# Kernel optimization log

Measured on AMD Instinct MI355X. Metric: run time of the kernel, lower is better.

The kernel has to match this reference:

```python
import jax, jax.numpy as jnp
import numpy as np

EPS = 1e-12  # torch F.normalize eps

def _l2n(x, axis):
    n = jnp.linalg.norm(x, axis=axis, keepdims=True)
    return x / jnp.maximum(n, EPS)

def setup_inputs() -> dict:
    key = jax.random.key(0)
    ks = jax.random.split(key, 11)
    B, N, D = 8, 4096, 512
    s = 1.0 / np.sqrt(D)
    return {
        'a': jax.random.normal(ks[0], (B, N, D), jnp.float32),
        'b': jax.random.normal(ks[1], (B, N, D), jnp.float32),
        'Wq': jax.random.normal(ks[2], (D, D), jnp.float32) * s,
        'bq': jax.random.normal(ks[3], (D,), jnp.float32) * s,
        'Wk': jax.random.normal(ks[4], (D, D), jnp.float32) * s,
        'bk': jax.random.normal(ks[5], (D,), jnp.float32) * s,
        'w_g': jax.random.normal(ks[6], (D, 1), jnp.float32),
        'Wp': jax.random.normal(ks[7], (D, D), jnp.float32) * s,
        'bp': jax.random.normal(ks[8], (D,), jnp.float32) * s,
        'Wf': jax.random.normal(ks[9], (D, D), jnp.float32) * s,
        'bf': jax.random.normal(ks[10], (D,), jnp.float32) * s,
    }

def reference(a, b, Wq, bq, Wk, bk, w_g, Wp, bp, Wf, bf):
    D = a.shape[-1]
    scale = D ** (-0.5)
    query = _l2n(jnp.einsum('bnd,ed->bne', a, Wq) + bq, axis=-1)   # [B,N,D]
    key = _l2n(jnp.einsum('bnd,ed->bne', b, Wk) + bk, axis=-1)     # [B,N,D]
    A = (query @ w_g) * scale                                      # [B,N,1]
    A = _l2n(A, axis=1)                                            # normalize over seq
    G = jnp.sum(A * query, axis=1)                                 # [B,D] learned pooling
    gk = G[:, None, :] * key                                       # broadcast [B,N,D]
    out = jnp.einsum('bnd,ed->bne', gk, Wp) + bp + query           # residual
    out = jnp.einsum('bnd,ed->bne', out, Wf) + bf
    return out
```

## Files before the change

### kernel.cpp

```cpp
#include <hip/hip_runtime.h>
#include <stdint.h>

#define DD 512
#define MTOT 32768

typedef float f32x4 __attribute__((ext_vector_type(4)));
typedef __bf16 bf16x8 __attribute__((ext_vector_type(8)));

static __device__ __forceinline__ unsigned short f2bf(float f) {
  union { float f; unsigned int u; } c; c.f = f;
  unsigned int r = c.u + 0x7fffu + ((c.u >> 16) & 1u);
  return (unsigned short)(r >> 16);
}
static __device__ __forceinline__ float bf2f(unsigned short h) {
  union { unsigned int u; float f; } c; c.u = ((unsigned int)h) << 16;
  return c.f;
}

union FragU { uint4 u; bf16x8 b; };

static __device__ __forceinline__ void load_lds16(const void* g, void* l) {
  __builtin_amdgcn_global_load_lds(
      (const __attribute__((address_space(1))) void*)g,
      (__attribute__((address_space(3))) void*)l, 16, 0, 0);
}

__global__ __launch_bounds__(256) void cvt3w_k(const float* __restrict__ W0,
    const float* __restrict__ W1, const float* __restrict__ W2,
    unsigned short* __restrict__ D0, unsigned short* __restrict__ D1,
    unsigned short* __restrict__ D2, float* __restrict__ stats) {
  int slab = blockIdx.x >> 8;
  if (slab == 3) {
    int i = ((blockIdx.x - 768) * 256 + threadIdx.x) * 4;
    *(float4*)(stats + i) = make_float4(0.f, 0.f, 0.f, 0.f);
    return;
  }
  int off = ((blockIdx.x & 255) * 256 + threadIdx.x) * 4;
  const float* s = slab == 0 ? W0 : slab == 1 ? W1 : W2;
  unsigned short* d = slab == 0 ? D0 : slab == 1 ? D1 : D2;
  float4 f = *(const float4*)(s + off);
  ushort4 h;
  h.x = f2bf(f.x); h.y = f2bf(f.y); h.z = f2bf(f.z); h.w = f2bf(f.w);
  *(ushort4*)(d + off) = h;
}

__global__ __launch_bounds__(256) void scalew_k(const float* __restrict__ Wp,
    const float* __restrict__ G, unsigned short* __restrict__ out) {
  int i = (blockIdx.x * 256 + threadIdx.x) * 4;
  int b = i >> 18;
  int rem = i & 262143;
  int d = rem & 511;
  float4 w = *(const float4*)(Wp + rem);
  float4 g = *(const float4*)(G + b * DD + d);
  ushort4 h;
  h.x = f2bf(w.x * g.x); h.y = f2bf(w.y * g.y);
  h.z = f2bf(w.z * g.z); h.w = f2bf(w.w * g.w);
  *(ushort4*)(out + i) = h;
}

static __device__ __forceinline__ void gemm_core(
    const unsigned short* __restrict__ X, const unsigned short* __restrict__ W,
    int row0, int col0, unsigned short* As, unsigned short* Bs,
    f32x4 (&acc)[4][4]) {
  const int tid = threadIdx.x;
  const int lane = tid & 63, wave = tid >> 6;
  const int sr = lane >> 3;
  const int scol = ((lane & 7) ^ sr) * 8;
  const unsigned short* Ag = X + (size_t)(row0 + wave * 32 + sr) * DD + scol;
  const unsigned short* Bg = W + (size_t)(col0 + wave * 32 + sr) * DD + scol;
  const int ldsb = wave * 32 * 64;
  const int fr = lane & 15, quad = lane >> 4;
  const int wr = (wave >> 1) * 64, wc = (wave & 1) * 64;
  const int sw0 = ((quad ^ (fr & 7)) * 8);
  const int sw1 = (((quad + 4) ^ (fr & 7)) * 8);

  for (int k0 = 0; k0 < DD; k0 += 64) {
#pragma unroll
    for (int q = 0; q < 4; q++) {
      load_lds16(Ag + (size_t)q * 8 * DD + k0, As + ldsb + q * 8 * 64);
      load_lds16(Bg + (size_t)q * 8 * DD + k0, Bs + ldsb + q * 8 * 64);
    }
    __syncthreads();
#pragma unroll
    for (int kk = 0; kk < 2; kk++) {
      const int sw = kk ? sw1 : sw0;
      bf16x8 af[4], bfr[4];
#pragma unroll
      for (int i = 0; i < 4; i++) {
        FragU u; u.u = *(const uint4*)&As[(wr + i * 16 + fr) * 64 + sw];
        af[i] = u.b;
      }
#pragma unroll
      for (int j = 0; j < 4; j++) {
        FragU u; u.u = *(const uint4*)&Bs[(wc + j * 16 + fr) * 64 + sw];
        bfr[j] = u.b;
      }
#pragma unroll
      for (int i = 0; i < 4; i++)
#pragma unroll
        for (int j = 0; j < 4; j++)
          acc[i][j] = __builtin_amdgcn_mfma_f32_16x16x32_bf16(af[i], bfr[j], acc[i][j], 0, 0, 0);
    }
    __syncthreads();
  }
}

__global__ __launch_bounds__(256) void gemm_qk_k(
    const float* __restrict__ Xa, const float* __restrict__ Xb,
    const unsigned short* __restrict__ Wqw, const unsigned short* __restrict__ Wkw,
    const float* __restrict__ bq, const float* __restrict__ bk,
    const float* __restrict__ wg,
    float* __restrict__ ssqQ, float* __restrict__ ssqK, float* __restrict__ Pdot,
    unsigned short* __restrict__ Cq, unsigned short* __restrict__ Ck) {
  __shared__ float AsF[128 * 64];
  __shared__ unsigned short Bs[128 * 64];
  const int swz = (blockIdx.x & 7) * 256 + (blockIdx.x >> 3);
  const int isK = swz >> 10;
  const int t = swz & 1023;
  const int row0 = (t >> 2) * 128, col0 = (t & 3) * 128;
  const float* X = isK ? Xb : Xa;
  const unsigned short* W = isK ? Wkw : Wqw;
  const float* bias = isK ? bk : bq;
  float* ssq = isK ? ssqK : ssqQ;
  unsigned short* C = isK ? Ck : Cq;

  const int lane = threadIdx.x & 63, wave = threadIdx.x >> 6;

  const int rl = lane >> 4;
  const int gsE = (lane & 15) ^ (rl << 1);
  const int gsO = gsE ^ 1;
  const float* AgE = X + (size_t)(row0 + wave * 32 + rl) * DD + gsE * 4;
  const float* AgO = X + (size_t)(row0 + wave * 32 + rl) * DD + gsO * 4;
  const int ldsA = wave * 2048;

  const int sr = lane >> 3;
  const int scol = ((lane & 7) ^ sr) * 8;
  const unsigned short* Bg = W + (size_t)(col0 + wave * 32 + sr) * DD + scol;
  const int ldsb = wave * 32 * 64;

  const int fr = lane & 15, quad = lane >> 4;
  const int wr = (wave >> 1) * 64, wc = (wave & 1) * 64;
  const int xorv = ((fr & 7) >> 2) | ((fr & 3) << 1);
  const int swB0 = ((quad ^ (fr & 7)) * 8);
  const int swB1 = (((quad + 4) ^ (fr & 7)) * 8);

  f32x4 acc[4][4] = {};

  for (int k0 = 0; k0 < DD; k0 += 64) {
#pragma unroll
    for (int q = 0; q < 8; q++) {
      const float* src = ((q & 1) ? AgO : AgE) + (size_t)q * 4 * DD + k0;
      load_lds16(src, AsF + ldsA + q * 256);
    }
#pragma unroll
    for (int q = 0; q < 4; q++)
      load_lds16(Bg + (size_t)q * 8 * DD + k0, Bs + ldsb + q * 8 * 64);
    __syncthreads();
#pragma unroll
    for (int kk = 0; kk < 2; kk++) {
      const int glo = ((kk * 4 + quad) * 2) ^ xorv;
      const int ghi = glo ^ 1;
      const int swB = kk ? swB1 : swB0;
      bf16x8 af[4], bfr[4];
#pragma unroll
      for (int i = 0; i < 4; i++) {
        const float* ap = &AsF[(wr + i * 16 + fr) * 64];
        f32x4 lo = *(const f32x4*)(ap + glo * 4);
        f32x4 hi = *(const f32x4*)(ap + ghi * 4);
        bf16x8 v;
        v[0] = (__bf16)lo.x; v[1] = (__bf16)lo.y;
        v[2] = (__bf16)lo.z; v[3] = (__bf16)lo.w;
        v[4] = (__bf16)hi.x; v[5] = (__bf16)hi.y;
        v[6] = (__bf16)hi.z; v[7] = (__bf16)hi.w;
        af[i] = v;
      }
#pragma unroll
      for (int j = 0; j < 4; j++) {
        FragU u; u.u = *(const uint4*)&Bs[(wc + j * 16 + fr) * 64 + swB];
        bfr[j] = u.b;
      }
#pragma unroll
      for (int i = 0; i < 4; i++)
#pragma unroll
        for (int j = 0; j < 4; j++)
          acc[i][j] = __builtin_amdgcn_mfma_f32_16x16x32_bf16(af[i], bfr[j], acc[i][j], 0, 0, 0);
    }
    __syncthreads();
  }

  const int colbase = col0 + wc + fr;
  float bv4[4], wg4[4];
#pragma unroll
  for (int j = 0; j < 4; j++) bv4[j] = bias[colbase + j * 16];
  if (!isK) {
#pragma unroll
    for (int j = 0; j < 4; j++) wg4[j] = wg[colbase + j * 16];
  }
#pragma unroll
  for (int i = 0; i < 4; i++) {
#pragma unroll
    for (int r = 0; r < 4; r++) {
      const int row = row0 + wr + i * 16 + quad * 4 + r;
      float ssum = 0.f, dsum = 0.f;
#pragma unroll
      for (int j = 0; j < 4; j++) {
        size_t idx = (size_t)row * DD + colbase + j * 16;
        float v = acc[i][j][r] + bv4[j];
        C[idx] = f2bf(v);
        ssum += v * v;
        if (!isK) dsum += v * wg4[j];
      }
#pragma unroll
      for (int m = 1; m < 16; m <<= 1) ssum += __shfl_xor(ssum, m, 64);
      if (!isK) {
#pragma unroll
        for (int m = 1; m < 16; m <<= 1) dsum += __shfl_xor(dsum, m, 64);
      }
      if (fr == 0) {
        atomicAdd(&ssq[row], ssum);
        if (!isK) atomicAdd(&Pdot[row], dsum);
      }
    }
  }
}

template<int BBATCH, int EMODE>
__global__ __launch_bounds__(256) void gemm_k(
    const unsigned short* __restrict__ X,
    const unsigned short* __restrict__ Wb,
    const float* __restrict__ bias,
    const unsigned short* __restrict__ Qadd,
    const float* __restrict__ qinv,
    const float* __restrict__ kinv,
    void* __restrict__ Cv) {
  __shared__ unsigned short As[128 * 64];
  __shared__ unsigned short Bs[128 * 64];
  const int swz = (blockIdx.x & 7) * 128 + (blockIdx.x >> 3);
  const int row0 = (swz >> 2) * 128, col0 = (swz & 3) * 128;
  const unsigned short* W = Wb + (BBATCH ? (size_t)(row0 >> 12) * 262144 : 0);

  f32x4 acc[4][4] = {};
  gemm_core(X, W, row0, col0, As, Bs, acc);

  const int lane = threadIdx.x & 63, wave = threadIdx.x >> 6;
  const int fr = lane & 15, quad = lane >> 4;
  const int wr = (wave >> 1) * 64, wc = (wave & 1) * 64;
  const int colbase = col0 + wc + fr;
  float bv4[4];
#pragma unroll
  for (int j = 0; j < 4; j++) bv4[j] = bias[colbase + j * 16];
#pragma unroll
  for (int i = 0; i < 4; i++) {
#pragma unroll
    for (int r = 0; r < 4; r++) {
      const int row = row0 + wr + i * 16 + quad * 4 + r;
      float ki = 1.f, qi = 1.f;
      if (EMODE == 3) { ki = kinv[row]; qi = qinv[row]; }
#pragma unroll
      for (int j = 0; j < 4; j++) {
        size_t idx = (size_t)row * DD + colbase + j * 16;
        if (EMODE == 3) {
          float v = acc[i][j][r] * ki + bv4[j] + qi * bf2f(Qadd[idx]);
          ((unsigned short*)Cv)[idx] = f2bf(v);
        } else {
          ((float*)Cv)[idx] = acc[i][j][r] + bv4[j];
        }
      }
    }
  }
}

__global__ __launch_bounds__(256) void pool2_k(
    const float* __restrict__ ssqQ, const float* __restrict__ ssqK,
    const float* __restrict__ P, float* __restrict__ qinv,
    float* __restrict__ kinv, const unsigned short* __restrict__ Q,
    float* __restrict__ G) {
  const int b = blockIdx.x >> 5, chunk = blockIdx.x & 31;
  const int t = threadIdx.x, lane = t & 63, wave = t >> 6;
  __shared__ float sred[4];
  __shared__ float gred[4][512];

  float ss = 0.f;
  for (int i = t; i < 4096; i += 256) {
    int n = b * 4096 + i;
    float qi = 1.0f / fmaxf(sqrtf(ssqQ[n]), 1e-12f);
    float A = P[n] * qi;
    ss += A * A;
  }
#pragma unroll
  for (int m = 1; m < 64; m <<= 1) ss += __shfl_xor(ss, m, 64);
  if (lane == 0) sred[wave] = ss;
  if (t < 128) {
    int n = b * 4096 + chunk * 128 + t;
    qinv[n] = 1.0f / fmaxf(sqrtf(ssqQ[n]), 1e-12f);
    kinv[n] = 1.0f / fmaxf(sqrtf(ssqK[n]), 1e-12f);
  }
  __syncthreads();
  const float sinv_b =
      1.0f / fmaxf(sqrtf(sred[0] + sred[1] + sred[2] + sred[3]), 1e-12f);

  float acc[8] = {};
  const int r0 = b * 4096 + chunk * 128 + wave * 32;
  for (int r = 0; r < 32; r++) {
    const int n = r0 + r;
    float qi = 1.0f / fmaxf(sqrtf(ssqQ[n]), 1e-12f);
    float wrow = P[n] * qi * qi * sinv_b;
    uint4 u = *(const uint4*)(Q + (size_t)n * DD + lane * 8);
    const unsigned short* h = (const unsigned short*)&u;
#pragma unroll
    for (int j = 0; j < 8; j++) acc[j] += wrow * bf2f(h[j]);
  }
#pragma unroll
  for (int j = 0; j < 8; j++) gred[wave][lane * 8 + j] = acc[j];
  __syncthreads();
  float g0 = gred[0][t] + gred[1][t] + gred[2][t] + gred[3][t];
  float g1 = gred[0][t + 256] + gred[1][t + 256] + gred[2][t + 256] + gred[3][t + 256];
  atomicAdd(&G[b * DD + t], g0);
  atomicAdd(&G[b * DD + t + 256], g1);
}

extern "C" void kernel_launch(void* const* d_in, const int* in_sizes, int n_in,
                              void* d_out, int out_size, void* d_ws, size_t ws_size,
                              hipStream_t stream) {
  const float* a   = (const float*)d_in[0];
  const float* b   = (const float*)d_in[1];
  const float* Wq  = (const float*)d_in[2];
  const float* bq  = (const float*)d_in[3];
  const float* Wk  = (const float*)d_in[4];
  const float* bk  = (const float*)d_in[5];
  const float* wg  = (const float*)d_in[6];
  const float* Wp  = (const float*)d_in[7];
  const float* bp  = (const float*)d_in[8];
  const float* Wf  = (const float*)d_in[9];
  const float* bfb = (const float*)d_in[10];

  const size_t WELEM = 262144;
  const size_t MD = (size_t)MTOT * DD;

  unsigned short* O1b = (unsigned short*)d_ws;
  unsigned short* Qb  = O1b + MD;
  unsigned short* Kb  = Qb + MD;
  unsigned short* Wqb = Kb + MD;
  unsigned short* Wkb = Wqb + WELEM;
  unsigned short* Wfb = Wkb + WELEM;
  unsigned short* Wps = Wfb + WELEM;
  float* stats = (float*)(Wps + 8 * WELEM);
  float* ssqQ  = stats;
  float* ssqK  = stats + MTOT;
  float* Pd    = stats + 2 * MTOT;
  float* G     = stats + 3 * MTOT;
  float* qinv  = G + 4096;
  float* kinv  = qinv + MTOT;

  cvt3w_k<<<dim3(868), dim3(256), 0, stream>>>(Wq, Wk, Wf, Wqb, Wkb, Wfb, stats);
  gemm_qk_k<<<dim3(2048), dim3(256), 0, stream>>>(
      a, b, Wqb, Wkb, bq, bk, wg, ssqQ, ssqK, Pd, Qb, Kb);
  pool2_k<<<dim3(256), dim3(256), 0, stream>>>(ssqQ, ssqK, Pd, qinv, kinv, Qb, G);
  scalew_k<<<dim3(2048), dim3(256), 0, stream>>>(Wp, G, Wps);
  gemm_k<1, 3><<<dim3(1024), dim3(256), 0, stream>>>(
      Kb, Wps, bp, Qb, qinv, kinv, O1b);
  gemm_k<0, 4><<<dim3(1024), dim3(256), 0, stream>>>(
      O1b, Wfb, bfb, nullptr, nullptr, nullptr, d_out);
}
```

Baseline: 308.0 us.

## Double-buffer QK GEMM with register-staged bf16 conversion of A tiles

The Q/K projection GEMM now loads fp32 A tiles from global memory into registers, converts them to bf16 and stores them into a double-buffered LDS tile. B tiles are also double-buffered through direct global-to-LDS loads. The next k-tile's loads are issued before the current tile's MFMAs, so memory latency can overlap compute and the loop needs one barrier per tile instead of two. Converting once at store time also halves LDS footprint and read traffic for A, at the cost of more registers and a possible drop in occupancy.

```diff
diff --git a/kernel.cpp b/kernel.cpp
--- a/kernel.cpp
+++ b/kernel.cpp
@@ -112,8 +112,8 @@
     const float* __restrict__ wg,
     float* __restrict__ ssqQ, float* __restrict__ ssqK, float* __restrict__ Pdot,
     unsigned short* __restrict__ Cq, unsigned short* __restrict__ Ck) {
-  __shared__ float AsF[128 * 64];
-  __shared__ unsigned short Bs[128 * 64];
+  __shared__ unsigned short Asm[2][128 * 64];
+  __shared__ unsigned short Bsm[2][128 * 64];
   const int swz = (blockIdx.x & 7) * 256 + (blockIdx.x >> 3);
   const int isK = swz >> 10;
   const int t = swz & 1023;
@@ -126,67 +126,98 @@
 
   const int lane = threadIdx.x & 63, wave = threadIdx.x >> 6;
 
-  const int rl = lane >> 4;
-  const int gsE = (lane & 15) ^ (rl << 1);
-  const int gsO = gsE ^ 1;
-  const float* AgE = X + (size_t)(row0 + wave * 32 + rl) * DD + gsE * 4;
-  const float* AgO = X + (size_t)(row0 + wave * 32 + rl) * DD + gsO * 4;
-  const int ldsA = wave * 2048;
+  const int arow = lane >> 3;
+  const int g = lane & 7;
+  const float* Af = X + (size_t)(row0 + wave * 32 + arow) * DD + g * 8;
+  const int awrb = wave * 2048 + arow * 64 + ((g ^ arow) * 8);
 
   const int sr = lane >> 3;
   const int scol = ((lane & 7) ^ sr) * 8;
   const unsigned short* Bg = W + (size_t)(col0 + wave * 32 + sr) * DD + scol;
-  const int ldsb = wave * 32 * 64;
+  const int ldsb = wave * 2048;
 
   const int fr = lane & 15, quad = lane >> 4;
   const int wr = (wave >> 1) * 64, wc = (wave & 1) * 64;
-  const int xorv = ((fr & 7) >> 2) | ((fr & 3) << 1);
-  const int swB0 = ((quad ^ (fr & 7)) * 8);
-  const int swB1 = (((quad + 4) ^ (fr & 7)) * 8);
+  const int sw0 = ((quad ^ (fr & 7)) * 8);
+  const int sw1 = (((quad + 4) ^ (fr & 7)) * 8);
+
+  unsigned short* As0 = Asm[0]; unsigned short* As1 = Asm[1];
+  unsigned short* Bs0 = Bsm[0]; unsigned short* Bs1 = Bsm[1];
 
   f32x4 acc[4][4] = {};
-
-  for (int k0 = 0; k0 < DD; k0 += 64) {
-#pragma unroll
-    for (int q = 0; q < 8; q++) {
-      const float* src = ((q & 1) ? AgO : AgE) + (size_t)q * 4 * DD + k0;
-      load_lds16(src, AsF + ldsA + q * 256);
-    }
-#pragma unroll
-    for (int q = 0; q < 4; q++)
-      load_lds16(Bg + (size_t)q * 8 * DD + k0, Bs + ldsb + q * 8 * 64);
+  f32x4 aA0[4], aA1[4], aB0[4], aB1[4];
+
+#define LOAD_A(R0, R1, K0)                                        \
+  do {                                                            \
+    _Pragma("unroll") for (int q = 0; q < 4; q++) {               \
+      const float* s_ = Af + (size_t)q * 8 * DD + (K0);           \
+      R0[q] = *(const f32x4*)s_;                                  \
+      R1[q] = *(const f32x4*)(s_ + 4);                            \
+    }                                                             \
+  } while (0)
+
+#define STORE_A(R0, R1, AS)                                       \
+  do {                                                            \
+    _Pragma("unroll") for (int q = 0; q < 4; q++) {               \
+      union { uint4 u4; unsigned short h[8]; } pk_;               \
+      pk_.h[0] = f2bf(R0[q].x); pk_.h[1] = f2bf(R0[q].y);         \
+      pk_.h[2] = f2bf(R0[q].z); pk_.h[3] = f2bf(R0[q].w);         \
+      pk_.h[4] = f2bf(R1[q].x); pk_.h[5] = f2bf(R1[q].y);         \
+      pk_.h[6] = f2bf(R1[q].z); pk_.h[7] = f2bf(R1[q].w);         \
+      *(uint4*)&(AS)[awrb + q * 512] = pk_.u4;                    \
+    }                                                             \
+  } while (0)
+
+#define LOAD_B(K0, BS)                                            \
+  do {                                                            \
+    _Pragma("unroll") for (int q = 0; q < 4; q++)                 \
+      load_lds16(Bg + (size_t)q * 8 * DD + (K0), (BS) + ldsb + q * 512); \
+  } while (0)
+
+#define COMPUTE(AS, BS)                                           \
+  do {                                                            \
+    _Pragma("unroll") for (int kk = 0; kk < 2; kk++) {            \
+      const int sw = kk ? sw1 : sw0;                              \
+      bf16x8 af[4], bfr[4];                                       \
+      _Pragma("unroll") for (int i = 0; i < 4; i++) {             \
+        FragU u; u.u = *(const uint4*)&(AS)[(wr + i * 16 + fr) * 64 + sw]; \
+        af[i] = u.b;                                              \
+      }                                                           \
+      _Pragma("unroll") for (int j = 0; j < 4; j++) {             \
+        FragU u; u.u = *(const uint4*)&(BS)[(wc + j * 16 + fr) * 64 + sw]; \
+        bfr[j] = u.b;                                             \
+      }                                                           \
+      _Pragma("unroll") for (int i = 0; i < 4; i++)               \
+        _Pragma("unroll") for (int j = 0; j < 4; j++)             \
+          acc[i][j] = __builtin_amdgcn_mfma_f32_16x16x32_bf16(    \
+              af[i], bfr[j], acc[i][j], 0, 0, 0);                 \
+    }                                                             \
+  } while (0)
+
+  LOAD_A(aA0, aA1, 0);
+  LOAD_B(0, Bs0);
+  STORE_A(aA0, aA1, As0);
+  __syncthreads();
+
+#pragma unroll
+  for (int k0 = 0; k0 < 512; k0 += 128) {
+    LOAD_A(aB0, aB1, k0 + 64);
+    LOAD_B(k0 + 64, Bs1);
+    COMPUTE(As0, Bs0);
+    STORE_A(aB0, aB1, As1);
     __syncthreads();
-#pragma unroll
-    for (int kk = 0; kk < 2; kk++) {
-      const int glo = ((kk * 4 + quad) * 2) ^ xorv;
-      const int ghi = glo ^ 1;
-      const int swB = kk ? swB1 : swB0;
-      bf16x8 af[4], bfr[4];
-#pragma unroll
-      for (int i = 0; i < 4; i++) {
-        const float* ap = &AsF[(wr + i * 16 + fr) * 64];
-        f32x4 lo = *(const f32x4*)(ap + glo * 4);
-        f32x4 hi = *(const f32x4*)(ap + ghi * 4);
-        bf16x8 v;
-        v[0] = (__bf16)lo.x; v[1] = (__bf16)lo.y;
-        v[2] = (__bf16)lo.z; v[3] = (__bf16)lo.w;
-        v[4] = (__bf16)hi.x; v[5] = (__bf16)hi.y;
-        v[6] = (__bf16)hi.z; v[7] = (__bf16)hi.w;
-        af[i] = v;
-      }
-#pragma unroll
-      for (int j = 0; j < 4; j++) {
-        FragU u; u.u = *(const uint4*)&Bs[(wc + j * 16 + fr) * 64 + swB];
-        bfr[j] = u.b;
-      }
-#pragma unroll
-      for (int i = 0; i < 4; i++)
-#pragma unroll
-        for (int j = 0; j < 4; j++)
-          acc[i][j] = __builtin_amdgcn_mfma_f32_16x16x32_bf16(af[i], bfr[j], acc[i][j], 0, 0, 0);
-    }
+    if (k0 < 384) {
+      LOAD_A(aA0, aA1, k0 + 128);
+      LOAD_B(k0 + 128, Bs0);
+    }
+    COMPUTE(As1, Bs1);
+    if (k0 < 384) STORE_A(aA0, aA1, As0);
     __syncthreads();
   }
+#undef LOAD_A
+#undef STORE_A
+#undef LOAD_B
+#undef COMPUTE
 
   const int colbase = col0 + wc + fr;
   float bv4[4], wg4[4];
```

Measured after the change: 335.7 us. 9.0% more time.

## Fuse all stages into one persistent megakernel with software grid barriers

Applied to the files above, without the earlier changes.

Replaces the six separate kernel launches with a single persistent kernel of 512 blocks that walks through weight conversion, QK GEMM, pooling, Wp scaling and the two output GEMMs, separated by atomic-counter grid barriers. Stats and the barrier counter are zeroed with a memset beforehand. The aim is to remove per-launch overhead and tail gaps between kernels. In exchange, occupancy is capped at 512 blocks (launch bounds 256,2), GEMM tiles loop inside each block, and the grid barriers add spin-wait cost and rely on every block being co-resident.

```diff
diff --git a/kernel.cpp b/kernel.cpp
--- a/kernel.cpp
+++ b/kernel.cpp
@@ -3,6 +3,7 @@
 
 #define DD 512
 #define MTOT 32768
+#define NBLK 512
 
 typedef float f32x4 __attribute__((ext_vector_type(4)));
 typedef __bf16 bf16x8 __attribute__((ext_vector_type(8)));
@@ -25,37 +26,216 @@
       (__attribute__((address_space(3))) void*)l, 16, 0, 0);
 }
 
-__global__ __launch_bounds__(256) void cvt3w_k(const float* __restrict__ W0,
-    const float* __restrict__ W1, const float* __restrict__ W2,
-    unsigned short* __restrict__ D0, unsigned short* __restrict__ D1,
-    unsigned short* __restrict__ D2, float* __restrict__ stats) {
-  int slab = blockIdx.x >> 8;
-  if (slab == 3) {
-    int i = ((blockIdx.x - 768) * 256 + threadIdx.x) * 4;
-    *(float4*)(stats + i) = make_float4(0.f, 0.f, 0.f, 0.f);
-    return;
-  }
-  int off = ((blockIdx.x & 255) * 256 + threadIdx.x) * 4;
-  const float* s = slab == 0 ? W0 : slab == 1 ? W1 : W2;
-  unsigned short* d = slab == 0 ? D0 : slab == 1 ? D1 : D2;
+static __device__ __forceinline__ void grid_bar(unsigned* bar) {
+  __syncthreads();
+  if (threadIdx.x == 0) {
+    unsigned* cnt = bar;
+    unsigned* gen = bar + 1;
+    __threadfence();
+    unsigned g = __hip_atomic_load(gen, __ATOMIC_RELAXED, __HIP_MEMORY_SCOPE_AGENT);
+    unsigned a = __hip_atomic_fetch_add(cnt, 1u, __ATOMIC_ACQ_REL, __HIP_MEMORY_SCOPE_AGENT);
+    if (a == NBLK - 1) {
+      __hip_atomic_store(cnt, 0u, __ATOMIC_RELAXED, __HIP_MEMORY_SCOPE_AGENT);
+      __hip_atomic_fetch_add(gen, 1u, __ATOMIC_ACQ_REL, __HIP_MEMORY_SCOPE_AGENT);
+    } else {
+      while (__hip_atomic_load(gen, __ATOMIC_ACQUIRE, __HIP_MEMORY_SCOPE_AGENT) == g)
+        __builtin_amdgcn_s_sleep(2);
+    }
+    __threadfence();
+  }
+  __syncthreads();
+}
+
+struct MegaP {
+  const float *a, *b, *Wq, *bq, *Wk, *bk, *wg, *Wp, *bp, *Wf, *bfb;
+  unsigned short *O1b, *Qb, *Kb, *Wqb, *Wkb, *Wfb, *Wps;
+  float *ssqQ, *ssqK, *Pd, *G, *qinv, *kinv;
+  float *out;
+  unsigned* bar;
+};
+
+static __device__ __forceinline__ void cvt_unit(const MegaP& P, int u) {
+  const int tid = threadIdx.x;
+  int slab = u >> 8;
+  int off = ((u & 255) * 256 + tid) * 4;
+  const float* s = slab == 0 ? P.Wq : slab == 1 ? P.Wk : P.Wf;
+  unsigned short* d = slab == 0 ? P.Wqb : slab == 1 ? P.Wkb : P.Wfb;
   float4 f = *(const float4*)(s + off);
   ushort4 h;
   h.x = f2bf(f.x); h.y = f2bf(f.y); h.z = f2bf(f.z); h.w = f2bf(f.w);
   *(ushort4*)(d + off) = h;
 }
 
-__global__ __launch_bounds__(256) void scalew_k(const float* __restrict__ Wp,
-    const float* __restrict__ G, unsigned short* __restrict__ out) {
-  int i = (blockIdx.x * 256 + threadIdx.x) * 4;
+static __device__ void qk_tile(const MegaP& P, int t, unsigned char* smem) {
+  float* AsF = (float*)smem;
+  unsigned short* Bs = (unsigned short*)(smem + 32768);
+  const int swz = (t & 7) * 256 + (t >> 3);
+  const int isK = swz >> 10;
+  const int tt = swz & 1023;
+  const int row0 = (tt >> 2) * 128, col0 = (tt & 3) * 128;
+  const float* X = isK ? P.b : P.a;
+  const unsigned short* W = isK ? P.Wkb : P.Wqb;
+  const float* bias = isK ? P.bk : P.bq;
+  float* ssq = isK ? P.ssqK : P.ssqQ;
+  unsigned short* C = isK ? P.Kb : P.Qb;
+
+  const int lane = threadIdx.x & 63, wave = threadIdx.x >> 6;
+
+  const int rl = lane >> 4;
+  const int gsE = (lane & 15) ^ (rl << 1);
+  const int gsO = gsE ^ 1;
+  const float* AgE = X + (size_t)(row0 + wave * 32 + rl) * DD + gsE * 4;
+  const float* AgO = X + (size_t)(row0 + wave * 32 + rl) * DD + gsO * 4;
+  const int ldsA = wave * 2048;
+
+  const int sr = lane >> 3;
+  const int scol = ((lane & 7) ^ sr) * 8;
+  const unsigned short* Bg = W + (size_t)(col0 + wave * 32 + sr) * DD + scol;
+  const int ldsb = wave * 2048;
+
+  const int fr = lane & 15, quad = lane >> 4;
+  const int wr = (wave >> 1) * 64, wc = (wave & 1) * 64;
+  const int xorv = ((fr & 7) >> 2) | ((fr & 3) << 1);
+  const int swB0 = ((quad ^ (fr & 7)) * 8);
+  const int swB1 = (((quad + 4) ^ (fr & 7)) * 8);
+
+  f32x4 acc[4][4] = {};
+
+  for (int k0 = 0; k0 < DD; k0 += 64) {
+#pragma unroll
+    for (int q = 0; q < 8; q++) {
+      const float* src = ((q & 1) ? AgO : AgE) + (size_t)q * 4 * DD + k0;
+      load_lds16(src, AsF + ldsA + q * 256);
+    }
+#pragma unroll
+    for (int q = 0; q < 4; q++)
+      load_lds16(Bg + (size_t)q * 8 * DD + k0, Bs + ldsb + q * 512);
+    __syncthreads();
+#pragma unroll
+    for (int kk = 0; kk < 2; kk++) {
+      const int glo = ((kk * 4 + quad) * 2) ^ xorv;
+      const int ghi = glo ^ 1;
+      const int swB = kk ? swB1 : swB0;
+      bf16x8 af[4], bfr[4];
+#pragma unroll
+      for (int i = 0; i < 4; i++) {
+        const float* ap = &AsF[(wr + i * 16 + fr) * 64];
+        f32x4 lo = *(const f32x4*)(ap + glo * 4);
+        f32x4 hi = *(const f32x4*)(ap + ghi * 4);
+        bf16x8 v;
+        v[0] = (__bf16)lo.x; v[1] = (__bf16)lo.y;
+        v[2] = (__bf16)lo.z; v[3] = (__bf16)lo.w;
+        v[4] = (__bf16)hi.x; v[5] = (__bf16)hi.y;
+        v[6] = (__bf16)hi.z; v[7] = (__bf16)hi.w;
+        af[i] = v;
+      }
+#pragma unroll
+      for (int j = 0; j < 4; j++) {
+        FragU u; u.u = *(const uint4*)&Bs[(wc + j * 16 + fr) * 64 + swB];
+        bfr[j] = u.b;
+      }
+#pragma unroll
+      for (int i = 0; i < 4; i++)
+#pragma unroll
+        for (int j = 0; j < 4; j++)
+          acc[i][j] = __builtin_amdgcn_mfma_f32_16x16x32_bf16(af[i], bfr[j], acc[i][j], 0, 0, 0);
+    }
+    __syncthreads();
+  }
+
+  const int colbase = col0 + wc + fr;
+  float bv4[4], wg4[4];
+#pragma unroll
+  for (int j = 0; j < 4; j++) bv4[j] = bias[colbase + j * 16];
+  if (!isK) {
+#pragma unroll
+    for (int j = 0; j < 4; j++) wg4[j] = P.wg[colbase + j * 16];
+  }
+#pragma unroll
+  for (int i = 0; i < 4; i++) {
+#pragma unroll
+    for (int r = 0; r < 4; r++) {
+      const int row = row0 + wr + i * 16 + quad * 4 + r;
+      float ssum = 0.f, dsum = 0.f;
+#pragma unroll
+      for (int j = 0; j < 4; j++) {
+        size_t idx = (size_t)row * DD + colbase + j * 16;
+        float v = acc[i][j][r] + bv4[j];
+        C[idx] = f2bf(v);
+        ssum += v * v;
+        if (!isK) dsum += v * wg4[j];
+      }
+#pragma unroll
+      for (int m = 1; m < 16; m <<= 1) ssum += __shfl_xor(ssum, m, 64);
+      if (!isK) {
+#pragma unroll
+        for (int m = 1; m < 16; m <<= 1) dsum += __shfl_xor(dsum, m, 64);
+      }
+      if (fr == 0) {
+        atomicAdd(&ssq[row], ssum);
+        if (!isK) atomicAdd(&P.Pd[row], dsum);
+      }
+    }
+  }
+}
+
+static __device__ void pool_unit(const MegaP& P, int u, unsigned char* smem) {
+  float* sred = (float*)smem;
+  float* gred = (float*)(smem + 64);
+  const int b = u >> 6, chunk = u & 63;
+  const int t = threadIdx.x, lane = t & 63, wave = t >> 6;
+
+  float ss = 0.f;
+  for (int i = t; i < 4096; i += 256) {
+    int n = b * 4096 + i;
+    float qi = 1.0f / fmaxf(sqrtf(P.ssqQ[n]), 1e-12f);
+    float A = P.Pd[n] * qi;
+    ss += A * A;
+  }
+#pragma unroll
+  for (int m = 1; m < 64; m <<= 1) ss += __shfl_xor(ss, m, 64);
+  if (lane == 0) sred[wave] = ss;
+  if (t < 64) {
+    int n = b * 4096 + chunk * 64 + t;
+    P.qinv[n] = 1.0f / fmaxf(sqrtf(P.ssqQ[n]), 1e-12f);
+    P.kinv[n] = 1.0f / fmaxf(sqrtf(P.ssqK[n]), 1e-12f);
+  }
+  __syncthreads();
+  const float sinv_b =
+      1.0f / fmaxf(sqrtf(sred[0] + sred[1] + sred[2] + sred[3]), 1e-12f);
+
+  float acc[8] = {};
+  const int r0 = b * 4096 + chunk * 64 + wave * 16;
+  for (int r = 0; r < 16; r++) {
+    const int n = r0 + r;
+    float qi = 1.0f / fmaxf(sqrtf(P.ssqQ[n]), 1e-12f);
+    float wrow = P.Pd[n] * qi * qi * sinv_b;
+    uint4 uu = *(const uint4*)(P.Qb + (size_t)n * DD + lane * 8);
+    const unsigned short* h = (const unsigned short*)&uu;
+#pragma unroll
+    for (int j = 0; j < 8; j++) acc[j] += wrow * bf2f(h[j]);
+  }
+#pragma unroll
+  for (int j = 0; j < 8; j++) gred[wave * 512 + lane * 8 + j] = acc[j];
+  __syncthreads();
+  float g0 = gred[t] + gred[512 + t] + gred[1024 + t] + gred[1536 + t];
+  float g1 = gred[t + 256] + gred[512 + t + 256] + gred[1024 + t + 256] + gred[1536 + t + 256];
+  atomicAdd(&P.G[b * DD + t], g0);
+  atomicAdd(&P.G[b * DD + t + 256], g1);
+  __syncthreads();
+}
+
+static __device__ __forceinline__ void scalew_unit(const MegaP& P, int u) {
+  int i = (u * 256 + threadIdx.x) * 4;
   int b = i >> 18;
   int rem = i & 262143;
   int d = rem & 511;
-  float4 w = *(const float4*)(Wp + rem);
-  float4 g = *(const float4*)(G + b * DD + d);
+  float4 w = *(const float4*)(P.Wp + rem);
+  float4 g = *(const float4*)(P.G + b * DD + d);
   ushort4 h;
   h.x = f2bf(w.x * g.x); h.y = f2bf(w.y * g.y);
   h.z = f2bf(w.z * g.z); h.w = f2bf(w.w * g.w);
-  *(ushort4*)(out + i) = h;
+  *(ushort4*)(P.Wps + i) = h;
 }
 
 static __device__ __forceinline__ void gemm_core(
@@ -68,7 +248,7 @@
   const int scol = ((lane & 7) ^ sr) * 8;
   const unsigned short* Ag = X + (size_t)(row0 + wave * 32 + sr) * DD + scol;
   const unsigned short* Bg = W + (size_t)(col0 + wave * 32 + sr) * DD + scol;
-  const int ldsb = wave * 32 * 64;
+  const int ldsb = wave * 2048;
   const int fr = lane & 15, quad = lane >> 4;
   const int wr = (wave >> 1) * 64, wc = (wave & 1) * 64;
   const int sw0 = ((quad ^ (fr & 7)) * 8);
@@ -77,8 +257,8 @@
   for (int k0 = 0; k0 < DD; k0 += 64) {
 #pragma unroll
     for (int q = 0; q < 4; q++) {
-      load_lds16(Ag + (size_t)q * 8 * DD + k0, As + ldsb + q * 8 * 64);
-      load_lds16(Bg + (size_t)q * 8 * DD + k0, Bs + ldsb + q * 8 * 64);
+      load_lds16(Ag + (size_t)q * 8 * DD + k0, As + ldsb + q * 512);
+      load_lds16(Bg + (size_t)q * 8 * DD + k0, Bs + ldsb + q * 512);
     }
     __syncthreads();
 #pragma unroll
@@ -105,139 +285,16 @@
   }
 }
 
-__global__ __launch_bounds__(256) void gemm_qk_k(
-    const float* __restrict__ Xa, const float* __restrict__ Xb,
-    const unsigned short* __restrict__ Wqw, const unsigned short* __restrict__ Wkw,
-    const float* __restrict__ bq, const float* __restrict__ bk,
-    const float* __restrict__ wg,
-    float* __restrict__ ssqQ, float* __restrict__ ssqK, float* __restrict__ Pdot,
-    unsigned short* __restrict__ Cq, unsigned short* __restrict__ Ck) {
-  __shared__ float AsF[128 * 64];
-  __shared__ unsigned short Bs[128 * 64];
-  const int swz = (blockIdx.x & 7) * 256 + (blockIdx.x >> 3);
-  const int isK = swz >> 10;
-  const int t = swz & 1023;
-  const int row0 = (t >> 2) * 128, col0 = (t & 3) * 128;
-  const float* X = isK ? Xb : Xa;
-  const unsigned short* W = isK ? Wkw : Wqw;
-  const float* bias = isK ? bk : bq;
-  float* ssq = isK ? ssqK : ssqQ;
-  unsigned short* C = isK ? Ck : Cq;
-
-  const int lane = threadIdx.x & 63, wave = threadIdx.x >> 6;
-
-  const int rl = lane >> 4;
-  const int gsE = (lane & 15) ^ (rl << 1);
-  const int gsO = gsE ^ 1;
-  const float* AgE = X + (size_t)(row0 + wave * 32 + rl) * DD + gsE * 4;
-  const float* AgO = X + (size_t)(row0 + wave * 32 + rl) * DD + gsO * 4;
-  const int ldsA = wave * 2048;
-
-  const int sr = lane >> 3;
-  const int scol = ((lane & 7) ^ sr) * 8;
-  const unsigned short* Bg = W + (size_t)(col0 + wave * 32 + sr) * DD + scol;
-  const int ldsb = wave * 32 * 64;
-
-  const int fr = lane & 15, quad = lane >> 4;
-  const int wr = (wave >> 1) * 64, wc = (wave & 1) * 64;
-  const int xorv = ((fr & 7) >> 2) | ((fr & 3) << 1);
-  const int swB0 = ((quad ^ (fr & 7)) * 8);
-  const int swB1 = (((quad + 4) ^ (fr & 7)) * 8);
-
-  f32x4 acc[4][4] = {};
-
-  for (int k0 = 0; k0 < DD; k0 += 64) {
-#pragma unroll
-    for (int q = 0; q < 8; q++) {
-      const float* src = ((q & 1) ? AgO : AgE) + (size_t)q * 4 * DD + k0;
-      load_lds16(src, AsF + ldsA + q * 256);
-    }
-#pragma unroll
-    for (int q = 0; q < 4; q++)
-      load_lds16(Bg + (size_t)q * 8 * DD + k0, Bs + ldsb + q * 8 * 64);
-    __syncthreads();
-#pragma unroll
-    for (int kk = 0; kk < 2; kk++) {
-      const int glo = ((kk * 4 + quad) * 2) ^ xorv;
-      const int ghi = glo ^ 1;
-      const int swB = kk ? swB1 : swB0;
-      bf16x8 af[4], bfr[4];
-#pragma unroll
-      for (int i = 0; i < 4; i++) {
-        const float* ap = &AsF[(wr + i * 16 + fr) * 64];
-        f32x4 lo = *(const f32x4*)(ap + glo * 4);
-        f32x4 hi = *(const f32x4*)(ap + ghi * 4);
-        bf16x8 v;
-        v[0] = (__bf16)lo.x; v[1] = (__bf16)lo.y;
-        v[2] = (__bf16)lo.z; v[3] = (__bf16)lo.w;
-        v[4] = (__bf16)hi.x; v[5] = (__bf16)hi.y;
-        v[6] = (__bf16)hi.z; v[7] = (__bf16)hi.w;
-        af[i] = v;
-      }
-#pragma unroll
-      for (int j = 0; j < 4; j++) {
-        FragU u; u.u = *(const uint4*)&Bs[(wc + j * 16 + fr) * 64 + swB];
-        bfr[j] = u.b;
-      }
-#pragma unroll
-      for (int i = 0; i < 4; i++)
-#pragma unroll
-        for (int j = 0; j < 4; j++)
-          acc[i][j] = __builtin_amdgcn_mfma_f32_16x16x32_bf16(af[i], bfr[j], acc[i][j], 0, 0, 0);
-    }
-    __syncthreads();
-  }
-
-  const int colbase = col0 + wc + fr;
-  float bv4[4], wg4[4];
-#pragma unroll
-  for (int j = 0; j < 4; j++) bv4[j] = bias[colbase + j * 16];
-  if (!isK) {
-#pragma unroll
-    for (int j = 0; j < 4; j++) wg4[j] = wg[colbase + j * 16];
-  }
-#pragma unroll
-  for (int i = 0; i < 4; i++) {
-#pragma unroll
-    for (int r = 0; r < 4; r++) {
-      const int row = row0 + wr + i * 16 + quad * 4 + r;
-      float ssum = 0.f, dsum = 0.f;
-#pragma unroll
-      for (int j = 0; j < 4; j++) {
-        size_t idx = (size_t)row * DD + colbase + j * 16;
-        float v = acc[i][j][r] + bv4[j];
-        C[idx] = f2bf(v);
-        ssum += v * v;
-        if (!isK) dsum += v * wg4[j];
-      }
-#pragma unroll
-      for (int m = 1; m < 16; m <<= 1) ssum += __shfl_xor(ssum, m, 64);
-      if (!isK) {
-#pragma unroll
-        for (int m = 1; m < 16; m <<= 1) dsum += __shfl_xor(dsum, m, 64);
-      }
-      if (fr == 0) {
-        atomicAdd(&ssq[row], ssum);
-        if (!isK) atomicAdd(&Pdot[row], dsum);
-      }
-    }
-  }
-}
-
-template<int BBATCH, int EMODE>
-__global__ __launch_bounds__(256) void gemm_k(
-    const unsigned short* __restrict__ X,
-    const unsigned short* __restrict__ Wb,
-    const float* __restrict__ bias,
-    const unsigned short* __restrict__ Qadd,
-    const float* __restrict__ qinv,
-    const float* __restrict__ kinv,
-    void* __restrict__ Cv) {
-  __shared__ unsigned short As[128 * 64];
-  __shared__ unsigned short Bs[128 * 64];
-  const int swz = (blockIdx.x & 7) * 128 + (blockIdx.x >> 3);
+template<int EMODE>
+static __device__ void gemm_tile(const MegaP& P, int t, unsigned char* smem) {
+  unsigned short* As = (unsigned short*)smem;
+  unsigned short* Bs = (unsigned short*)(smem + 16384);
+  const int swz = (t & 7) * 128 + (t >> 3);
   const int row0 = (swz >> 2) * 128, col0 = (swz & 3) * 128;
-  const unsigned short* W = Wb + (BBATCH ? (size_t)(row0 >> 12) * 262144 : 0);
+  const unsigned short* X = (EMODE == 3) ? P.Kb : P.O1b;
+  const unsigned short* W = (EMODE == 3)
+      ? P.Wps + (size_t)(row0 >> 12) * 262144 : P.Wfb;
+  const float* bias = (EMODE == 3) ? P.bp : P.bfb;
 
   f32x4 acc[4][4] = {};
   gemm_core(X, W, row0, col0, As, Bs, acc);
@@ -255,85 +312,46 @@
     for (int r = 0; r < 4; r++) {
       const int row = row0 + wr + i * 16 + quad * 4 + r;
       float ki = 1.f, qi = 1.f;
-      if (EMODE == 3) { ki = kinv[row]; qi = qinv[row]; }
+      if (EMODE == 3) { ki = P.kinv[row]; qi = P.qinv[row]; }
 #pragma unroll
       for (int j = 0; j < 4; j++) {
         size_t idx = (size_t)row * DD + colbase + j * 16;
         if (EMODE == 3) {
-          float v = acc[i][j][r] * ki + bv4[j] + qi * bf2f(Qadd[idx]);
-          ((unsigned short*)Cv)[idx] = f2bf(v);
+          float v = acc[i][j][r] * ki + bv4[j] + qi * bf2f(P.Qb[idx]);
+          P.O1b[idx] = f2bf(v);
         } else {
-          ((float*)Cv)[idx] = acc[i][j][r] + bv4[j];
+          P.out[idx] = acc[i][j][r] + bv4[j];
         }
       }
     }
   }
-}
-
-__global__ __launch_bounds__(256) void pool2_k(
-    const float* __restrict__ ssqQ, const float* __restrict__ ssqK,
-    const float* __restrict__ P, float* __restrict__ qinv,
-    float* __restrict__ kinv, const unsigned short* __restrict__ Q,
-    float* __restrict__ G) {
-  const int b = blockIdx.x >> 5, chunk = blockIdx.x & 31;
-  const int t = threadIdx.x, lane = t & 63, wave = t >> 6;
-  __shared__ float sred[4];
-  __shared__ float gred[4][512];
-
-  float ss = 0.f;
-  for (int i = t; i < 4096; i += 256) {
-    int n = b * 4096 + i;
-    float qi = 1.0f / fmaxf(sqrtf(ssqQ[n]), 1e-12f);
-    float A = P[n] * qi;
-    ss += A * A;
-  }
-#pragma unroll
-  for (int m = 1; m < 64; m <<= 1) ss += __shfl_xor(ss, m, 64);
-  if (lane == 0) sred[wave] = ss;
-  if (t < 128) {
-    int n = b * 4096 + chunk * 128 + t;
-    qinv[n] = 1.0f / fmaxf(sqrtf(ssqQ[n]), 1e-12f);
-    kinv[n] = 1.0f / fmaxf(sqrtf(ssqK[n]), 1e-12f);
-  }
-  __syncthreads();
-  const float sinv_b =
-      1.0f / fmaxf(sqrtf(sred[0] + sred[1] + sred[2] + sred[3]), 1e-12f);
-
-  float acc[8] = {};
-  const int r0 = b * 4096 + chunk * 128 + wave * 32;
-  for (int r = 0; r < 32; r++) {
-    const int n = r0 + r;
-    float qi = 1.0f / fmaxf(sqrtf(ssqQ[n]), 1e-12f);
-    float wrow = P[n] * qi * qi * sinv_b;
-    uint4 u = *(const uint4*)(Q + (size_t)n * DD + lane * 8);
-    const unsigned short* h = (const unsigned short*)&u;
-#pragma unroll
-    for (int j = 0; j < 8; j++) acc[j] += wrow * bf2f(h[j]);
-  }
-#pragma unroll
-  for (int j = 0; j < 8; j++) gred[wave][lane * 8 + j] = acc[j];
-  __syncthreads();
-  float g0 = gred[0][t] + gred[1][t] + gred[2][t] + gred[3][t];
-  float g1 = gred[0][t + 256] + gred[1][t + 256] + gred[2][t + 256] + gred[3][t + 256];
-  atomicAdd(&G[b * DD + t], g0);
-  atomicAdd(&G[b * DD + t + 256], g1);
+  __syncthreads();
+}
+
+__global__ __launch_bounds__(256, 2) void mega_k(MegaP P) {
+  __shared__ __align__(16) unsigned char smem[49152];
+  const int bid = blockIdx.x;
+
+  for (int u = bid; u < 768; u += NBLK) cvt_unit(P, u);
+  grid_bar(P.bar);
+#pragma unroll 1
+  for (int i = 0; i < 4; i++) qk_tile(P, bid + NBLK * i, smem);
+  grid_bar(P.bar);
+  pool_unit(P, bid, smem);
+  grid_bar(P.bar);
+#pragma unroll 1
+  for (int i = 0; i < 4; i++) scalew_unit(P, bid + NBLK * i);
+  grid_bar(P.bar);
+#pragma unroll 1
+  for (int i = 0; i < 2; i++) gemm_tile<3>(P, bid + NBLK * i, smem);
+  grid_bar(P.bar);
+#pragma unroll 1
+  for (int i = 0; i < 2; i++) gemm_tile<4>(P, bid + NBLK * i, smem);
 }
 
 extern "C" void kernel_launch(void* const* d_in, const int* in_sizes, int n_in,
                               void* d_out, int out_size, void* d_ws, size_t ws_size,
                               hipStream_t stream) {
-  const float* a   = (const float*)d_in[0];
-  const float* b   = (const float*)d_in[1];
-  const float* Wq  = (const float*)d_in[2];
-  const float* bq  = (const float*)d_in[3];
-  const float* Wk  = (const float*)d_in[4];
-  const float* bk  = (const float*)d_in[5];
-  const float* wg  = (const float*)d_in[6];
-  const float* Wp  = (const float*)d_in[7];
-  const float* bp  = (const float*)d_in[8];
-  const float* Wf  = (const float*)d_in[9];
-  const float* bfb = (const float*)d_in[10];
-
   const size_t WELEM = 262144;
   const size_t MD = (size_t)MTOT * DD;
 
@@ -345,20 +363,30 @@
   unsigned short* Wfb = Wkb + WELEM;
   unsigned short* Wps = Wfb + WELEM;
   float* stats = (float*)(Wps + 8 * WELEM);
-  float* ssqQ  = stats;
-  float* ssqK  = stats + MTOT;
-  float* Pd    = stats + 2 * MTOT;
-  float* G     = stats + 3 * MTOT;
-  float* qinv  = G + 4096;
-  float* kinv  = qinv + MTOT;
-
-  cvt3w_k<<<dim3(868), dim3(256), 0, stream>>>(Wq, Wk, Wf, Wqb, Wkb, Wfb, stats);
-  gemm_qk_k<<<dim3(2048), dim3(256), 0, stream>>>(
-      a, b, Wqb, Wkb, bq, bk, wg, ssqQ, ssqK, Pd, Qb, Kb);
-  pool2_k<<<dim3(256), dim3(256), 0, stream>>>(ssqQ, ssqK, Pd, qinv, kinv, Qb, G);
-  scalew_k<<<dim3(2048), dim3(256), 0, stream>>>(Wp, G, Wps);
-  gemm_k<1, 3><<<dim3(1024), dim3(256), 0, stream>>>(
-      Kb, Wps, bp, Qb, qinv, kinv, O1b);
-  gemm_k<0, 4><<<dim3(1024), dim3(256), 0, stream>>>(
-      O1b, Wfb, bfb, nullptr, nullptr, nullptr, d_out);
-}
+
+  MegaP P;
+  P.a   = (const float*)d_in[0];
+  P.b   = (const float*)d_in[1];
+  P.Wq  = (const float*)d_in[2];
+  P.bq  = (const float*)d_in[3];
+  P.Wk  = (const float*)d_in[4];
+  P.bk  = (const float*)d_in[5];
+  P.wg  = (const float*)d_in[6];
+  P.Wp  = (const float*)d_in[7];
+  P.bp  = (const float*)d_in[8];
+  P.Wf  = (const float*)d_in[9];
+  P.bfb = (const float*)d_in[10];
+  P.O1b = O1b; P.Qb = Qb; P.Kb = Kb;
+  P.Wqb = Wqb; P.Wkb = Wkb; P.Wfb = Wfb; P.Wps = Wps;
+  P.ssqQ = stats;
+  P.ssqK = stats + MTOT;
+  P.Pd   = stats + 2 * MTOT;
+  P.G    = stats + 3 * MTOT;
+  P.bar  = (unsigned*)(P.G + 4096);
+  P.qinv = (float*)(P.bar + 2);
+  P.kinv = P.qinv + MTOT;
+  P.out  = (float*)d_out;
+
+  hipMemsetAsync(stats, 0, 102400 * sizeof(float) + 2 * sizeof(unsigned), stream);
+  mega_k<<<dim3(NBLK), dim3(256), 0, stream>>>(P);
+}
```

After: 800.8 us. +160.0%, slower.

## Fold Wp into Wf algebraically to merge the two trailing GEMMs

Applied to the files above, without the earlier changes.

Precomputes Wf·Wp (and the combined bias Wf·bp+bf) once, scales it per batch by G, and computes the output as one kernel that does K·M and Q·Wf back to back with a single fp32 epilogue. This removes the intermediate bf16 O1 buffer write/read and one kernel launch, and adds a small weight GEMM plus a transpose of Wp. The per-row GEMM FLOPs stay the same (two K=512 GEMMs per tile). The product is rounded to bf16 before use, which changes the rounding pattern.

```diff
diff --git a/kernel.cpp b/kernel.cpp
--- a/kernel.cpp
+++ b/kernel.cpp
@@ -27,35 +27,46 @@
 
 __global__ __launch_bounds__(256) void cvt3w_k(const float* __restrict__ W0,
     const float* __restrict__ W1, const float* __restrict__ W2,
+    const float* __restrict__ Wp,
     unsigned short* __restrict__ D0, unsigned short* __restrict__ D1,
-    unsigned short* __restrict__ D2, float* __restrict__ stats) {
-  int slab = blockIdx.x >> 8;
-  if (slab == 3) {
-    int i = ((blockIdx.x - 768) * 256 + threadIdx.x) * 4;
+    unsigned short* __restrict__ D2, unsigned short* __restrict__ WpT,
+    float* __restrict__ stats) {
+  __shared__ float tl[64][65];
+  const int u = blockIdx.x, t = threadIdx.x;
+  if (u < 768) {
+    int slab = u >> 8;
+    int off = ((u & 255) * 256 + t) * 4;
+    const float* s = slab == 0 ? W0 : slab == 1 ? W1 : W2;
+    unsigned short* d = slab == 0 ? D0 : slab == 1 ? D1 : D2;
+    float4 f = *(const float4*)(s + off);
+    ushort4 h;
+    h.x = f2bf(f.x); h.y = f2bf(f.y); h.z = f2bf(f.z); h.w = f2bf(f.w);
+    *(ushort4*)(d + off) = h;
+  } else if (u < 832) {
+    const int tile = u - 768, tr = tile >> 3, tc = tile & 7;
+    const int r = t >> 2, cq = t & 3;
+    const float* src = Wp + (size_t)(tr * 64 + r) * 512 + tc * 64 + cq * 16;
+#pragma unroll
+    for (int i = 0; i < 4; i++) {
+      float4 v = ((const float4*)src)[i];
+      tl[r][cq * 16 + i * 4 + 0] = v.x; tl[r][cq * 16 + i * 4 + 1] = v.y;
+      tl[r][cq * 16 + i * 4 + 2] = v.z; tl[r][cq * 16 + i * 4 + 3] = v.w;
+    }
+    __syncthreads();
+    unsigned short* dst = WpT + (size_t)(tc * 64 + r) * 512 + tr * 64 + cq * 16;
+#pragma unroll
+    for (int i = 0; i < 4; i++) {
+      ushort4 h;
+      h.x = f2bf(tl[cq * 16 + i * 4 + 0][r]);
+      h.y = f2bf(tl[cq * 16 + i * 4 + 1][r]);
+      h.z = f2bf(tl[cq * 16 + i * 4 + 2][r]);
+      h.w = f2bf(tl[cq * 16 + i * 4 + 3][r]);
+      ((ushort4*)dst)[i] = h;
+    }
+  } else {
+    int i = ((u - 832) * 256 + t) * 4;
     *(float4*)(stats + i) = make_float4(0.f, 0.f, 0.f, 0.f);
-    return;
-  }
-  int off = ((blockIdx.x & 255) * 256 + threadIdx.x) * 4;
-  const float* s = slab == 0 ? W0 : slab == 1 ? W1 : W2;
-  unsigned short* d = slab == 0 ? D0 : slab == 1 ? D1 : D2;
-  float4 f = *(const float4*)(s + off);
-  ushort4 h;
-  h.x = f2bf(f.x); h.y = f2bf(f.y); h.z = f2bf(f.z); h.w = f2bf(f.w);
-  *(ushort4*)(d + off) = h;
-}
-
-__global__ __launch_bounds__(256) void scalew_k(const float* __restrict__ Wp,
-    const float* __restrict__ G, unsigned short* __restrict__ out) {
-  int i = (blockIdx.x * 256 + threadIdx.x) * 4;
-  int b = i >> 18;
-  int rem = i & 262143;
-  int d = rem & 511;
-  float4 w = *(const float4*)(Wp + rem);
-  float4 g = *(const float4*)(G + b * DD + d);
-  ushort4 h;
-  h.x = f2bf(w.x * g.x); h.y = f2bf(w.y * g.y);
-  h.z = f2bf(w.z * g.z); h.w = f2bf(w.w * g.w);
-  *(ushort4*)(out + i) = h;
+  }
 }
 
 static __device__ __forceinline__ void gemm_core(
@@ -68,7 +79,7 @@
   const int scol = ((lane & 7) ^ sr) * 8;
   const unsigned short* Ag = X + (size_t)(row0 + wave * 32 + sr) * DD + scol;
   const unsigned short* Bg = W + (size_t)(col0 + wave * 32 + sr) * DD + scol;
-  const int ldsb = wave * 32 * 64;
+  const int ldsb = wave * 2048;
   const int fr = lane & 15, quad = lane >> 4;
   const int wr = (wave >> 1) * 64, wc = (wave & 1) * 64;
   const int sw0 = ((quad ^ (fr & 7)) * 8);
@@ -77,8 +88,8 @@
   for (int k0 = 0; k0 < DD; k0 += 64) {
 #pragma unroll
     for (int q = 0; q < 4; q++) {
-      load_lds16(Ag + (size_t)q * 8 * DD + k0, As + ldsb + q * 8 * 64);
-      load_lds16(Bg + (size_t)q * 8 * DD + k0, Bs + ldsb + q * 8 * 64);
+      load_lds16(Ag + (size_t)q * 8 * DD + k0, As + ldsb + q * 512);
+      load_lds16(Bg + (size_t)q * 8 * DD + k0, Bs + ldsb + q * 512);
     }
     __syncthreads();
 #pragma unroll
@@ -103,6 +114,55 @@
     }
     __syncthreads();
   }
+}
+
+__global__ __launch_bounds__(256) void fgemm_k(
+    const unsigned short* __restrict__ Wfb, const unsigned short* __restrict__ WpT,
+    const float* __restrict__ Wf, const float* __restrict__ bp,
+    const float* __restrict__ bfb, unsigned short* __restrict__ Fb,
+    float* __restrict__ bconst) {
+  const int bb = blockIdx.x, t = threadIdx.x;
+  if (bb >= 16) {
+    const int j = (bb - 16) * 128 + (t >> 1), half = t & 1;
+    float s = 0.f;
+    const float* wr = Wf + (size_t)j * 512 + half * 256;
+    const float* bpr = bp + half * 256;
+    for (int n = 0; n < 256; n++) s += wr[n] * bpr[n];
+    s += __shfl_xor(s, 1, 64);
+    if (half == 0) bconst[j] = s + bfb[j];
+    return;
+  }
+  __shared__ unsigned short As[128 * 64];
+  __shared__ unsigned short Bs[128 * 64];
+  const int row0 = (bb >> 2) * 128, col0 = (bb & 3) * 128;
+  f32x4 acc[4][4] = {};
+  gemm_core(Wfb, WpT, row0, col0, As, Bs, acc);
+  const int lane = t & 63, wave = t >> 6;
+  const int fr = lane & 15, quad = lane >> 4;
+  const int wr = (wave >> 1) * 64, wc = (wave & 1) * 64;
+#pragma unroll
+  for (int i = 0; i < 4; i++)
+#pragma unroll
+    for (int r = 0; r < 4; r++) {
+      const int row = row0 + wr + i * 16 + quad * 4 + r;
+#pragma unroll
+      for (int j = 0; j < 4; j++)
+        Fb[(size_t)row * 512 + col0 + wc + j * 16 + fr] = f2bf(acc[i][j][r]);
+    }
+}
+
+__global__ __launch_bounds__(256) void mscale_k(const unsigned short* __restrict__ Fb,
+    const float* __restrict__ G, unsigned short* __restrict__ Mb) {
+  int i = (blockIdx.x * 256 + threadIdx.x) * 4;
+  int b = i >> 18;
+  int rem = i & 262143;
+  int k = rem & 511;
+  ushort4 f = *(const ushort4*)(Fb + rem);
+  float4 g = *(const float4*)(G + b * DD + k);
+  ushort4 h;
+  h.x = f2bf(bf2f(f.x) * g.x); h.y = f2bf(bf2f(f.y) * g.y);
+  h.z = f2bf(bf2f(f.z) * g.z); h.w = f2bf(bf2f(f.w) * g.w);
+  *(ushort4*)(Mb + i) = h;
 }
 
 __global__ __launch_bounds__(256) void gemm_qk_k(
@@ -116,8 +176,8 @@
   __shared__ unsigned short Bs[128 * 64];
   const int swz = (blockIdx.x & 7) * 256 + (blockIdx.x >> 3);
   const int isK = swz >> 10;
-  const int t = swz & 1023;
-  const int row0 = (t >> 2) * 128, col0 = (t & 3) * 128;
+  const int tt = swz & 1023;
+  const int row0 = (tt >> 2) * 128, col0 = (tt & 3) * 128;
   const float* X = isK ? Xb : Xa;
   const unsigned short* W = isK ? Wkw : Wqw;
   const float* bias = isK ? bk : bq;
@@ -136,7 +196,7 @@
   const int sr = lane >> 3;
   const int scol = ((lane & 7) ^ sr) * 8;
   const unsigned short* Bg = W + (size_t)(col0 + wave * 32 + sr) * DD + scol;
-  const int ldsb = wave * 32 * 64;
+  const int ldsb = wave * 2048;
 
   const int fr = lane & 15, quad = lane >> 4;
   const int wr = (wave >> 1) * 64, wc = (wave & 1) * 64;
@@ -154,7 +214,7 @@
     }
 #pragma unroll
     for (int q = 0; q < 4; q++)
-      load_lds16(Bg + (size_t)q * 8 * DD + k0, Bs + ldsb + q * 8 * 64);
+      load_lds16(Bg + (size_t)q * 8 * DD + k0, Bs + ldsb + q * 512);
     __syncthreads();
 #pragma unroll
     for (int kk = 0; kk < 2; kk++) {
@@ -224,52 +284,6 @@
   }
 }
 
-template<int BBATCH, int EMODE>
-__global__ __launch_bounds__(256) void gemm_k(
-    const unsigned short* __restrict__ X,
-    const unsigned short* __restrict__ Wb,
-    const float* __restrict__ bias,
-    const unsigned short* __restrict__ Qadd,
-    const float* __restrict__ qinv,
-    const float* __restrict__ kinv,
-    void* __restrict__ Cv) {
-  __shared__ unsigned short As[128 * 64];
-  __shared__ unsigned short Bs[128 * 64];
-  const int swz = (blockIdx.x & 7) * 128 + (blockIdx.x >> 3);
-  const int row0 = (swz >> 2) * 128, col0 = (swz & 3) * 128;
-  const unsigned short* W = Wb + (BBATCH ? (size_t)(row0 >> 12) * 262144 : 0);
-
-  f32x4 acc[4][4] = {};
-  gemm_core(X, W, row0, col0, As, Bs, acc);
-
-  const int lane = threadIdx.x & 63, wave = threadIdx.x >> 6;
-  const int fr = lane & 15, quad = lane >> 4;
-  const int wr = (wave >> 1) * 64, wc = (wave & 1) * 64;
-  const int colbase = col0 + wc + fr;
-  float bv4[4];
-#pragma unroll
-  for (int j = 0; j < 4; j++) bv4[j] = bias[colbase + j * 16];
-#pragma unroll
-  for (int i = 0; i < 4; i++) {
-#pragma unroll
-    for (int r = 0; r < 4; r++) {
-      const int row = row0 + wr + i * 16 + quad * 4 + r;
-      float ki = 1.f, qi = 1.f;
-      if (EMODE == 3) { ki = kinv[row]; qi = qinv[row]; }
-#pragma unroll
-      for (int j = 0; j < 4; j++) {
-        size_t idx = (size_t)row * DD + colbase + j * 16;
-        if (EMODE == 3) {
-          float v = acc[i][j][r] * ki + bv4[j] + qi * bf2f(Qadd[idx]);
-          ((unsigned short*)Cv)[idx] = f2bf(v);
-        } else {
-          ((float*)Cv)[idx] = acc[i][j][r] + bv4[j];
-        }
-      }
-    }
-  }
-}
-
 __global__ __launch_bounds__(256) void pool2_k(
     const float* __restrict__ ssqQ, const float* __restrict__ ssqK,
     const float* __restrict__ P, float* __restrict__ qinv,
@@ -317,6 +331,45 @@
   float g1 = gred[0][t + 256] + gred[1][t + 256] + gred[2][t + 256] + gred[3][t + 256];
   atomicAdd(&G[b * DD + t], g0);
   atomicAdd(&G[b * DD + t + 256], g1);
+}
+
+__global__ __launch_bounds__(256) void final_k(
+    const unsigned short* __restrict__ Kb, const unsigned short* __restrict__ Qb,
+    const unsigned short* __restrict__ Mb, const unsigned short* __restrict__ Wfb,
+    const float* __restrict__ bconst,
+    const float* __restrict__ qinv, const float* __restrict__ kinv,
+    float* __restrict__ out) {
+  __shared__ unsigned short As[128 * 64];
+  __shared__ unsigned short Bs[128 * 64];
+  const int swz = (blockIdx.x & 7) * 128 + (blockIdx.x >> 3);
+  const int row0 = (swz >> 2) * 128, col0 = (swz & 3) * 128;
+  const unsigned short* M = Mb + (size_t)(row0 >> 12) * 262144;
+
+  f32x4 accK[4][4] = {};
+  gemm_core(Kb, M, row0, col0, As, Bs, accK);
+  f32x4 accQ[4][4] = {};
+  gemm_core(Qb, Wfb, row0, col0, As, Bs, accQ);
+
+  const int lane = threadIdx.x & 63, wave = threadIdx.x >> 6;
+  const int fr = lane & 15, quad = lane >> 4;
+  const int wr = (wave >> 1) * 64, wc = (wave & 1) * 64;
+  const int colbase = col0 + wc + fr;
+  float bv4[4];
+#pragma unroll
+  for (int j = 0; j < 4; j++) bv4[j] = bconst[colbase + j * 16];
+#pragma unroll
+  for (int i = 0; i < 4; i++) {
+#pragma unroll
+    for (int r = 0; r < 4; r++) {
+      const int row = row0 + wr + i * 16 + quad * 4 + r;
+      const float ki = kinv[row], qi = qinv[row];
+#pragma unroll
+      for (int j = 0; j < 4; j++) {
+        size_t idx = (size_t)row * DD + colbase + j * 16;
+        out[idx] = accK[i][j][r] * ki + accQ[i][j][r] * qi + bv4[j];
+      }
+    }
+  }
 }
 
 extern "C" void kernel_launch(void* const* d_in, const int* in_sizes, int n_in,
@@ -337,28 +390,30 @@
   const size_t WELEM = 262144;
   const size_t MD = (size_t)MTOT * DD;
 
-  unsigned short* O1b = (unsigned short*)d_ws;
-  unsigned short* Qb  = O1b + MD;
+  unsigned short* Qb  = (unsigned short*)d_ws;
   unsigned short* Kb  = Qb + MD;
   unsigned short* Wqb = Kb + MD;
   unsigned short* Wkb = Wqb + WELEM;
   unsigned short* Wfb = Wkb + WELEM;
-  unsigned short* Wps = Wfb + WELEM;
-  float* stats = (float*)(Wps + 8 * WELEM);
+  unsigned short* WpT = Wfb + WELEM;
+  unsigned short* Fb  = WpT + WELEM;
+  unsigned short* Mb  = Fb + WELEM;
+  float* stats = (float*)(Mb + 8 * WELEM);
   float* ssqQ  = stats;
   float* ssqK  = stats + MTOT;
   float* Pd    = stats + 2 * MTOT;
   float* G     = stats + 3 * MTOT;
   float* qinv  = G + 4096;
   float* kinv  = qinv + MTOT;
-
-  cvt3w_k<<<dim3(868), dim3(256), 0, stream>>>(Wq, Wk, Wf, Wqb, Wkb, Wfb, stats);
+  float* bconst = kinv + MTOT;
+
+  cvt3w_k<<<dim3(932), dim3(256), 0, stream>>>(
+      Wq, Wk, Wf, Wp, Wqb, Wkb, Wfb, WpT, stats);
+  fgemm_k<<<dim3(20), dim3(256), 0, stream>>>(Wfb, WpT, Wf, bp, bfb, Fb, bconst);
   gemm_qk_k<<<dim3(2048), dim3(256), 0, stream>>>(
       a, b, Wqb, Wkb, bq, bk, wg, ssqQ, ssqK, Pd, Qb, Kb);
   pool2_k<<<dim3(256), dim3(256), 0, stream>>>(ssqQ, ssqK, Pd, qinv, kinv, Qb, G);
-  scalew_k<<<dim3(2048), dim3(256), 0, stream>>>(Wp, G, Wps);
-  gemm_k<1, 3><<<dim3(1024), dim3(256), 0, stream>>>(
-      Kb, Wps, bp, Qb, qinv, kinv, O1b);
-  gemm_k<0, 4><<<dim3(1024), dim3(256), 0, stream>>>(
-      O1b, Wfb, bfb, nullptr, nullptr, nullptr, d_out);
-}
+  mscale_k<<<dim3(2048), dim3(256), 0, stream>>>(Fb, G, Mb);
+  final_k<<<dim3(1024), dim3(256), 0, stream>>>(
+      Kb, Qb, Mb, Wfb, bconst, qinv, kinv, (float*)d_out);
+}
```

Result: slower. 336.8 us (+9.4%).
